# Optimization experiments

Measured on AMD Instinct MI355X. Metric: run time of the kernel, lower is better.

The kernel has to match this reference:

```python
import jax, jax.numpy as jnp
import numpy as np

B, L, IN, DM, DS, DC, EXP = 4, 1024, 256, 1024, 16, 4, 2
DI = EXP * DM            # d_inner = 2048
DTR = (DM + 15) // 16    # dt_rank = 64


def setup_inputs() -> dict:
    key = jax.random.key(0)
    ks = jax.random.split(key, 10)
    s = lambda k, sh, sc: jax.random.normal(k, sh, jnp.float32) * sc
    return {
        "x": s(ks[0], (B, L, IN), 1.0),
        "W_emb": s(ks[1], (DM, IN), IN ** -0.5),
        "b_emb": jnp.zeros((DM,), jnp.float32),
        "in_proj_w": s(ks[2], (2 * DI, DM), DM ** -0.5),
        "conv_w": s(ks[3], (DI, 1, DC), DC ** -0.5),
        "conv_b": jnp.zeros((DI,), jnp.float32),
        "x_proj_w": s(ks[4], (DTR + 2 * DS, DI), DI ** -0.5),
        "dt_proj_w": s(ks[5], (DI, DTR), DTR ** -0.5),
        "dt_proj_b": s(ks[6], (DI,), 0.1),
        "A_log": jnp.tile(jnp.log(jnp.arange(1, DS + 1, dtype=jnp.float32)), (DI, 1)),
        "D": jnp.ones((DI,), jnp.float32),
        "out_proj_w": s(ks[7], (DM, DI), DI ** -0.5),
        "fc_w": s(ks[8], (1, DM), DM ** -0.5),
        "fc_b": jnp.zeros((1,), jnp.float32),
    }


def _forward(x, W_emb, b_emb, in_proj_w, conv_w, conv_b, x_proj_w,
             dt_proj_w, dt_proj_b, A_log, D, out_proj_w, fc_w, fc_b):
    h = x @ W_emb.T + b_emb                      # [B,L,DM] input embedding
    xz = h @ in_proj_w.T                         # [B,L,2*DI]
    u, z = jnp.split(xz, 2, axis=-1)             # each [B,L,DI]
    # causal depthwise conv over time (pad left d_conv-1)
    uc = jax.lax.conv_general_dilated(
        u.transpose(0, 2, 1), conv_w, (1,), [(DC - 1, 0)],
        dimension_numbers=('NCH', 'OIH', 'NCH'), feature_group_count=DI)
    u = jax.nn.silu(uc.transpose(0, 2, 1) + conv_b)   # [B,L,DI]
    xdbl = u @ x_proj_w.T                        # [B,L,DTR+2*DS]
    dt, Bm, Cm = jnp.split(xdbl, [DTR, DTR + DS], axis=-1)
    delta = jax.nn.softplus(dt @ dt_proj_w.T + dt_proj_b)  # [B,L,DI]
    A = -jnp.exp(A_log)                          # [DI,DS]

    def step(hst, ins):
        d_t, B_t, C_t, u_t = ins                 # [B,DI],[B,DS],[B,DS],[B,DI]
        dA = jnp.exp(d_t[..., None] * A)         # [B,DI,DS]
        hst = dA * hst + (d_t * u_t)[..., None] * B_t[:, None, :]
        y = jnp.einsum('bds,bs->bd', hst, C_t)
        return hst, y

    h0 = jnp.zeros((B, DI, DS), u.dtype)
    _, ys = jax.lax.scan(step, h0, (delta.transpose(1, 0, 2),
                                    Bm.transpose(1, 0, 2),
                                    Cm.transpose(1, 0, 2),
                                    u.transpose(1, 0, 2)))
    y = ys.transpose(1, 0, 2) + D * u            # [B,L,DI] with D skip
    y = y * jax.nn.silu(z)                       # gate
    out = y @ out_proj_w.T                       # [B,L,DM]
    return out[:, -1, :] @ fc_w.T + fc_b         # [B,1]


def reference(x, W_emb, b_emb, in_proj_w, conv_w, conv_b, x_proj_w,
              dt_proj_w, dt_proj_b, A_log, D, out_proj_w, fc_w, fc_b):
    return _forward(x, W_emb, b_emb, in_proj_w, conv_w, conv_b, x_proj_w,
                    dt_proj_w, dt_proj_b, A_log, D, out_proj_w, fc_w, fc_b)
```

## Files before the change

kernel.cpp:

```cpp
#include <hip/hip_runtime.h>
#include <cstddef>
#include <cstdint>

namespace {

typedef _Float16 half8 __attribute__((ext_vector_type(8)));
typedef _Float16 half4 __attribute__((ext_vector_type(4)));
typedef float f32x4 __attribute__((ext_vector_type(4)));

constexpr int Bn   = 4;
constexpr int Ln   = 1024;
constexpr int INn  = 256;
constexpr int DMn  = 1024;
constexpr int DSn  = 16;
constexpr int DCn  = 4;
constexpr int DIn  = 2048;
constexpr int DTRn = 64;
constexpr int XPW  = DTRn + DSn;
constexpr int NCHUNK = 64;
constexpr int CHUNK  = Ln / NCHUNK;
constexpr int WCH  = 32;
constexpr int ML   = Bn * Ln;

__device__ __forceinline__ float silu_(float x) { return x / (1.f + __expf(-x)); }
__device__ __forceinline__ float softplus_(float x) {
    return fmaxf(x, 0.f) + __logf(1.f + __expf(-fabsf(x)));
}

__global__ __launch_bounds__(256)
void prep_mega(const float* __restrict__ x, _Float16* __restrict__ xh,
               const float* __restrict__ ip, _Float16* __restrict__ iph,
               const float* __restrict__ dtw, _Float16* __restrict__ dtwh,
               const float* __restrict__ W_emb, _Float16* __restrict__ W_embT,
               const float* __restrict__ x_proj, _Float16* __restrict__ xp_h,
               const float* __restrict__ fc_w, const float* __restrict__ out_w,
               float* __restrict__ wp,
               const float* __restrict__ b_emb, float* __restrict__ badd,
               const float* __restrict__ fc_b, float* __restrict__ out) {
    __shared__ float tile[32][33];
    const int bid = blockIdx.x, tid = threadIdx.x;
    if (bid < 4096) {
        const int n = bid;
        const float4 v = ((const float4*)ip)[n * 256 + tid];
        ((half4*)iph)[n * 256 + tid] =
            half4{(_Float16)v.x, (_Float16)v.y, (_Float16)v.z, (_Float16)v.w};
        const float4 bv = ((const float4*)b_emb)[tid];
        float s = v.x * bv.x + v.y * bv.y + v.z * bv.z + v.w * bv.w;
        for (int off = 32; off > 0; off >>= 1) s += __shfl_down(s, off);
        if ((tid & 63) == 0) tile[0][tid >> 6] = s;
        __syncthreads();
        if (tid == 0) badd[n] = tile[0][0] + tile[0][1] + tile[0][2] + tile[0][3];
    } else if (bid < 5248) {
        const float* in; _Float16* outp; int i;
        if (bid < 5120) { in = x;   outp = xh;   i = (bid - 4096) * 256 + tid; }
        else            { in = dtw; outp = dtwh; i = (bid - 5120) * 256 + tid; }
        const float4 v = ((const float4*)in)[i];
        ((half4*)outp)[i] = half4{(_Float16)v.x, (_Float16)v.y, (_Float16)v.z, (_Float16)v.w};
    } else if (bid < 5504) {
        const int bx = bid - 5248;
        const int m0 = (bx & 31) * 32, c0 = (bx >> 5) * 32;
        const int lc = tid & 31, lr = tid >> 5;
        #pragma unroll
        for (int ph = 0; ph < 4; ++ph)
            tile[lr + ph * 8][lc] = W_emb[(size_t)(m0 + lr + ph * 8) * INn + c0 + lc];
        __syncthreads();
        #pragma unroll
        for (int ph = 0; ph < 4; ++ph)
            W_embT[(size_t)(c0 + lr + ph * 8) * DMn + m0 + lc] = (_Float16)tile[lc][lr + ph * 8];
    } else if (bid < 5760) {
        const int i = (bid - 5504) * 256 + tid;
        const int r = i >> 9;
        const int c4 = i & 511;
        half4 h;
        if (r < XPW) {
            const float4 v = ((const float4*)(x_proj + (size_t)r * DIn))[c4];
            h = half4{(_Float16)v.x, (_Float16)v.y, (_Float16)v.z, (_Float16)v.w};
        } else {
            h = half4{(_Float16)0.f, (_Float16)0.f, (_Float16)0.f, (_Float16)0.f};
        }
        ((half4*)(xp_h + (size_t)r * DIn))[c4] = h;
    } else if (bid < 6016) {
        const int bx = bid - 5760;
        const int d = (bx & 7) * 256 + tid;
        const int c = bx >> 3;
        const int mstep = DMn / WCH;
        float s = 0.f;
        for (int m = c * mstep; m < (c + 1) * mstep; ++m)
            s += fc_w[m] * out_w[(size_t)m * DIn + d];
        wp[(size_t)c * DIn + d] = s;
    } else {
        if (tid < Bn) out[tid] = fc_b[0];
    }
}

__global__ __launch_bounds__(256)
void skgemm2(const _Float16* __restrict__ A, int lda,
             const _Float16* __restrict__ Bw, int ldb,
             float* __restrict__ P, int N, int Kc) {
    __shared__ _Float16 As[128 * 32];
    __shared__ _Float16 Bs[128 * 32];
    const int tid  = threadIdx.x;
    const int lane = tid & 63, wid = tid >> 6;
    const int wm = wid >> 1, wn = wid & 1;
    const int sk = blockIdx.x;
    const int m0 = blockIdx.y * 128;
    const int n0 = blockIdx.z * 128;
    const int M  = gridDim.y * 128;

    f32x4 acc[4][4] = {};
    const int kbeg = sk * Kc;
    for (int k0 = kbeg; k0 < kbeg + Kc; k0 += 32) {
        #pragma unroll
        for (int i = 0; i < 2; ++i) {
            const int off = tid * 16 + i * 4096;
            const int row = off >> 6;
            const int ch  = (off & 63) >> 1;
            const _Float16* ga = A  + (size_t)(m0 + row) * lda + k0 + ch;
            const _Float16* gb = Bw + (size_t)(n0 + row) * ldb + k0 + ch;
            __builtin_amdgcn_global_load_lds(
                (const __attribute__((address_space(1))) void*)ga,
                (__attribute__((address_space(3))) void*)(&As[off >> 1]), 16, 0, 0);
            __builtin_amdgcn_global_load_lds(
                (const __attribute__((address_space(1))) void*)gb,
                (__attribute__((address_space(3))) void*)(&Bs[off >> 1]), 16, 0, 0);
        }
        __syncthreads();
        const int ar = lane & 15;
        const int kq = (lane >> 4) * 8;
        half8 af[4], bf[4];
        #pragma unroll
        for (int i = 0; i < 4; ++i)
            af[i] = *(const half8*)&As[(wm * 64 + i * 16 + ar) * 32 + kq];
        #pragma unroll
        for (int j = 0; j < 4; ++j)
            bf[j] = *(const half8*)&Bs[(wn * 64 + j * 16 + ar) * 32 + kq];
        #pragma unroll
        for (int i = 0; i < 4; ++i)
            #pragma unroll
            for (int j = 0; j < 4; ++j)
                acc[i][j] = __builtin_amdgcn_mfma_f32_16x16x32_f16(af[i], bf[j], acc[i][j], 0, 0, 0);
        __syncthreads();
    }

    const int cr = (lane >> 4) * 4;
    const int cn = lane & 15;
    #pragma unroll
    for (int i = 0; i < 4; ++i) {
        #pragma unroll
        for (int j = 0; j < 4; ++j) {
            const int n = n0 + wn * 64 + j * 16 + cn;
            if (n < N) {
                #pragma unroll
                for (int r = 0; r < 4; ++r) {
                    const int m = m0 + wm * 64 + i * 16 + cr + r;
                    P[((size_t)sk * M + m) * N + n] = acc[i][j][r];
                }
            }
        }
    }
}

__global__ __launch_bounds__(256)
void skcomb(const float* __restrict__ P, _Float16* __restrict__ out, int total, int nsk) {
    const int i = blockIdx.x * 256 + threadIdx.x;
    if (i >= total) return;
    float s = 0.f;
    for (int k = 0; k < nsk; ++k) s += P[(size_t)k * total + i];
    out[i] = (_Float16)s;
}

__global__ __launch_bounds__(256)
void skcombB_clast(const float* __restrict__ P, _Float16* __restrict__ dtBh,
                   const _Float16* __restrict__ u, const float* __restrict__ x_proj,
                   float* __restrict__ Clast) {
    const int bid = blockIdx.x, tid = threadIdx.x;
    if (bid < 1280) {
        const int i = bid * 256 + tid;
        float s = 0.f;
        #pragma unroll
        for (int k = 0; k < 8; ++k) s += P[(size_t)k * (ML * XPW) + i];
        dtBh[i] = (_Float16)s;
    } else {
        const int wave = tid >> 6, lane = tid & 63;
        const int task = (bid - 1280) * 4 + wave;
        const int s_idx = task & 15, b = task >> 4;
        const _Float16* ur = u + ((size_t)b * Ln + (Ln - 1)) * DIn;
        const float* w = x_proj + (size_t)(XPW + s_idx) * DIn;
        float s = 0.f;
        for (int k = lane; k < DIn; k += 64) s += (float)ur[k] * w[k];
        for (int off = 32; off > 0; off >>= 1) s += __shfl_down(s, off);
        if (lane == 0) Clast[b * DSn + s_idx] = s;
    }
}

template<int ACT, bool HAS_BIAS>
__global__ __launch_bounds__(256)
void hgemm(const _Float16* __restrict__ A, int lda,
           const _Float16* __restrict__ Bw, int ldb,
           const float* __restrict__ bias,
           _Float16* __restrict__ Ch, int ldc,
           int N, int K) {
    __shared__ _Float16 As[128 * 32];
    __shared__ _Float16 Bs[128 * 32];
    const int tid  = threadIdx.x;
    const int lane = tid & 63, wid = tid >> 6;
    const int wm = wid >> 1, wn = wid & 1;
    const int m0 = blockIdx.y * 128, n0 = blockIdx.x * 128;

    f32x4 acc[4][4] = {};

    for (int k0 = 0; k0 < K; k0 += 32) {
        #pragma unroll
        for (int i = 0; i < 2; ++i) {
            const int off = tid * 16 + i * 4096;
            const int row = off >> 6;
            const int ch  = (off & 63) >> 1;
            const _Float16* ga = A  + (size_t)(m0 + row) * lda + k0 + ch;
            const _Float16* gb = Bw + (size_t)(n0 + row) * ldb + k0 + ch;
            __builtin_amdgcn_global_load_lds(
                (const __attribute__((address_space(1))) void*)ga,
                (__attribute__((address_space(3))) void*)(&As[off >> 1]), 16, 0, 0);
            __builtin_amdgcn_global_load_lds(
                (const __attribute__((address_space(1))) void*)gb,
                (__attribute__((address_space(3))) void*)(&Bs[off >> 1]), 16, 0, 0);
        }
        __syncthreads();

        const int ar = lane & 15;
        const int kq = (lane >> 4) * 8;
        half8 af[4], bf[4];
        #pragma unroll
        for (int i = 0; i < 4; ++i)
            af[i] = *(const half8*)&As[(wm * 64 + i * 16 + ar) * 32 + kq];
        #pragma unroll
        for (int j = 0; j < 4; ++j)
            bf[j] = *(const half8*)&Bs[(wn * 64 + j * 16 + ar) * 32 + kq];
        #pragma unroll
        for (int i = 0; i < 4; ++i)
            #pragma unroll
            for (int j = 0; j < 4; ++j)
                acc[i][j] = __builtin_amdgcn_mfma_f32_16x16x32_f16(af[i], bf[j], acc[i][j], 0, 0, 0);
        __syncthreads();
    }

    const int cr = (lane >> 4) * 4;
    const int cn = lane & 15;
    #pragma unroll
    for (int i = 0; i < 4; ++i) {
        #pragma unroll
        for (int j = 0; j < 4; ++j) {
            const int n = n0 + wn * 64 + j * 16 + cn;
            if (n < N) {
                #pragma unroll
                for (int r = 0; r < 4; ++r) {
                    const int m = m0 + wm * 64 + i * 16 + cr + r;
                    float v = acc[i][j][r];
                    if (HAS_BIAS) v += bias[n];
                    if (ACT == 1) v = softplus_(v);
                    Ch[(size_t)m * ldc + n] = (_Float16)v;
                }
            }
        }
    }
}

__global__ __launch_bounds__(256)
void conv_zlast(const _Float16* __restrict__ upre, const float* __restrict__ cw,
                const float* __restrict__ cb, _Float16* __restrict__ uh,
                const float* __restrict__ x, const _Float16* __restrict__ Wfh,
                const float* __restrict__ badd, float* __restrict__ zlast) {
    const int tid = threadIdx.x;
    const int bid = blockIdx.x;
    if (bid < 1024) {
        const int b  = bid >> 8;
        const int t0 = (bid & 255) * 4;
        const int d0 = tid * 8;
        const size_t rowbase = ((size_t)b * Ln + t0) * DIn + d0;

        half8 hzero;
        #pragma unroll
        for (int q = 0; q < 8; ++q) hzero[q] = (_Float16)0.f;

        half8 rows[7];
        if (t0 >= 3) {
            #pragma unroll
            for (int r = 0; r < 7; ++r)
                rows[r] = *(const half8*)(upre + rowbase + (ptrdiff_t)(r - 3) * DIn);
        } else {
            #pragma unroll
            for (int r = 0; r < 7; ++r) {
                const int t = t0 - 3 + r;
                rows[r] = (t >= 0) ? *(const half8*)(upre + rowbase + (ptrdiff_t)(r - 3) * DIn) : hzero;
            }
        }

        f32x4 cwq[8];
        float cbv[8];
        #pragma unroll
        for (int q = 0; q < 8; ++q) {
            cwq[q] = *(const f32x4*)(cw + (size_t)(d0 + q) * DCn);
            cbv[q] = cb[d0 + q];
        }

        #pragma unroll
        for (int s = 0; s < 4; ++s) {
            half8 o;
            #pragma unroll
            for (int q = 0; q < 8; ++q) {
                float acc = cbv[q];
                #pragma unroll
                for (int j = 0; j < DCn; ++j) acc += (float)rows[s + j][q] * cwq[q][j];
                o[q] = (_Float16)silu_(acc);
            }
            *(half8*)(uh + rowbase + (size_t)s * DIn) = o;
        }
    } else {
        const int task = (bid - 1024) * 256 + tid;
        const int j = task & (DIn - 1), b = task >> 11;
        const float4* x4 = (const float4*)(x + ((size_t)b * Ln + (Ln - 1)) * INn);
        const half4* w4 = (const half4*)(Wfh + (size_t)(DIn + j) * INn);
        float s = 0.f;
        #pragma unroll 8
        for (int q = 0; q < 64; ++q) {
            const float4 xv = x4[q];
            const half4 wv = w4[q];
            s += (float)wv[0] * xv.x + (float)wv[1] * xv.y
               + (float)wv[2] * xv.z + (float)wv[3] * xv.w;
        }
        zlast[(size_t)b * DIn + j] = s + badd[DIn + j];
    }
}

__global__ __launch_bounds__(256)
void scan_chunk_kernel(const _Float16* __restrict__ delta, const _Float16* __restrict__ u,
                       const _Float16* __restrict__ dtBh, const float* __restrict__ A_log,
                       float* __restrict__ cS, _Float16* __restrict__ cH) {
    const int d = blockIdx.x * 256 + threadIdx.x;
    const int c = blockIdx.y, b = blockIdx.z;
    float A[DSn], h[DSn];
    const float4* al = (const float4*)(A_log + (size_t)d * DSn);
    #pragma unroll
    for (int q = 0; q < 4; ++q) {
        const float4 v = al[q];
        A[q * 4 + 0] = -__expf(v.x); A[q * 4 + 1] = -__expf(v.y);
        A[q * 4 + 2] = -__expf(v.z); A[q * 4 + 3] = -__expf(v.w);
        h[q * 4 + 0] = 0.f; h[q * 4 + 1] = 0.f; h[q * 4 + 2] = 0.f; h[q * 4 + 3] = 0.f;
    }
    const float A0 = A[0];
    bool structured = true;
    #pragma unroll
    for (int s = 1; s < DSn; ++s)
        structured = structured && (fabsf(A[s] - (float)(s + 1) * A0) <= 1e-4f * (s + 1));

    float Ssum = 0.f;
    const size_t base = ((size_t)b * Ln + (size_t)c * CHUNK) * DIn + d;
    const _Float16* Bp = dtBh + ((size_t)b * Ln + (size_t)c * CHUNK) * XPW + DTRn;
    if (structured) {
        #pragma unroll 4
        for (int tt = 0; tt < CHUNK; ++tt) {
            const float dl = (float)delta[base + (size_t)tt * DIn];
            const float uu = (float)u[base + (size_t)tt * DIn];
            const float du = dl * uu;
            Ssum += dl;
            const half8 bv0 = *(const half8*)(Bp + tt * XPW);
            const half8 bv1 = *(const half8*)(Bp + tt * XPW + 8);
            float Bv[DSn];
            #pragma unroll
            for (int q = 0; q < 8; ++q) { Bv[q] = (float)bv0[q]; Bv[8 + q] = (float)bv1[q]; }
            const float e1 = __expf(dl * A0);
            const float e2 = e1 * e1, e4 = e2 * e2, e8 = e4 * e4;
            float E[DSn];
            E[0] = e1;      E[1] = e2;      E[2] = e2 * e1;  E[3] = e4;
            E[4] = e4 * e1; E[5] = e4 * e2; E[6] = E[5] * e1; E[7] = e8;
            E[8] = e8 * e1; E[9] = e8 * e2; E[10] = E[9] * e1; E[11] = e8 * e4;
            E[12] = E[11] * e1; E[13] = E[11] * e2; E[14] = E[13] * e1; E[15] = e8 * e8;
            #pragma unroll
            for (int s = 0; s < DSn; ++s) h[s] = E[s] * h[s] + du * Bv[s];
        }
    } else {
        #pragma unroll 4
        for (int tt = 0; tt < CHUNK; ++tt) {
            const float dl = (float)delta[base + (size_t)tt * DIn];
            const float uu = (float)u[base + (size_t)tt * DIn];
            const float du = dl * uu;
            Ssum += dl;
            const half8 bv0 = *(const half8*)(Bp + tt * XPW);
            const half8 bv1 = *(const half8*)(Bp + tt * XPW + 8);
            float Bv[DSn];
            #pragma unroll
            for (int q = 0; q < 8; ++q) { Bv[q] = (float)bv0[q]; Bv[8 + q] = (float)bv1[q]; }
            #pragma unroll
            for (int s = 0; s < DSn; ++s) h[s] = __expf(dl * A[s]) * h[s] + du * Bv[s];
        }
    }
    const size_t cidx = ((size_t)b * NCHUNK + c) * DIn + d;
    cS[cidx] = Ssum;
    half8 o0, o1;
    #pragma unroll
    for (int q = 0; q < 8; ++q) { o0[q] = (_Float16)h[q]; o1[q] = (_Float16)h[8 + q]; }
    *(half8*)(cH + cidx * DSn) = o0;
    *(half8*)(cH + cidx * DSn + 8) = o1;
}

__global__ __launch_bounds__(256)
void combine_v3(const float* __restrict__ cS, const _Float16* __restrict__ cH,
                const float* __restrict__ A_log, const float* __restrict__ Clast,
                const float* __restrict__ Dp, const _Float16* __restrict__ u,
                const float* __restrict__ zlast, const float* __restrict__ wp,
                float* __restrict__ out) {
    __shared__ float acc[16];
    const int tid = threadIdx.x;
    const int s = tid & 15;
    const int d = blockIdx.x * 16 + (tid >> 4);
    const int b = blockIdx.y;
    const float A = -__expf(A_log[(size_t)d * DSn + s]);
    float h = 0.f;
    const size_t cb0 = (size_t)b * NCHUNK;
    for (int c = 0; c < NCHUNK; ++c) {
        const size_t cidx = (cb0 + c) * DIn + d;
        h = __expf(A * cS[cidx]) * h + (float)cH[cidx * DSn + s];
    }
    float y = h * Clast[b * DSn + s];
    y += __shfl_xor(y, 1);
    y += __shfl_xor(y, 2);
    y += __shfl_xor(y, 4);
    y += __shfl_xor(y, 8);
    if (s == 0) {
        const float ul = (float)u[((size_t)b * Ln + (Ln - 1)) * DIn + d];
        float yy = y + Dp[d] * ul;
        yy *= silu_(zlast[(size_t)b * DIn + d]);
        float w = 0.f;
        #pragma unroll
        for (int c = 0; c < WCH; ++c) w += wp[(size_t)c * DIn + d];
        acc[tid >> 4] = yy * w;
    }
    __syncthreads();
    if (tid == 0) {
        float t = 0.f;
        #pragma unroll
        for (int i = 0; i < 16; ++i) t += acc[i];
        atomicAdd(&out[b], t);
    }
}

}

extern "C" void kernel_launch(void* const* d_in, const int* in_sizes, int n_in,
                              void* d_out, int out_size, void* d_ws, size_t ws_size,
                              hipStream_t stream) {
    (void)in_sizes; (void)n_in; (void)out_size; (void)ws_size;
    const float* x       = (const float*)d_in[0];
    const float* W_emb   = (const float*)d_in[1];
    const float* b_emb   = (const float*)d_in[2];
    const float* in_proj = (const float*)d_in[3];
    const float* conv_w  = (const float*)d_in[4];
    const float* conv_b  = (const float*)d_in[5];
    const float* x_proj  = (const float*)d_in[6];
    const float* dt_w    = (const float*)d_in[7];
    const float* dt_b    = (const float*)d_in[8];
    const float* A_log   = (const float*)d_in[9];
    const float* Dp      = (const float*)d_in[10];
    const float* out_w   = (const float*)d_in[11];
    const float* fc_w    = (const float*)d_in[12];
    const float* fc_b    = (const float*)d_in[13];
    float* out = (float*)d_out;
    char* w8 = (char*)d_ws;

    const size_t MB = 1ull << 20;
    _Float16* upreh    = (_Float16*)(w8);
    _Float16* uh       = (_Float16*)(w8 + 16 * MB);
    float*    wfoldP   = (float*)(w8 + 32 * MB);
    _Float16* deltah   = (_Float16*)(w8 + 32 * MB);
    float*    skp      = (float*)(w8 + 48 * MB);
    float*    cS       = skp;
    _Float16* cH       = (_Float16*)(w8 + 50 * MB);
    _Float16* dtBh     = (_Float16*)(w8 + 67 * MB);
    _Float16* xh       = (_Float16*)(w8 + 68 * MB);
    _Float16* W_embT_h = (_Float16*)(w8 + 70 * MB);
    _Float16* in_projh = (_Float16*)(w8 + 71 * MB);
    _Float16* xp_h     = (_Float16*)(w8 + 79 * MB);
    _Float16* dt_wh    = (_Float16*)(w8 + 80 * MB);
    _Float16* Wfoldh   = (_Float16*)(w8 + 81 * MB);
    float*    wp       = (float*)(w8 + 83 * MB);
    float*    badd     = (float*)(w8 + 84 * MB);
    float*    zlast    = badd + 4096;
    float*    Clast    = zlast + (size_t)Bn * DIn;

    prep_mega<<<6017, 256, 0, stream>>>(x, xh, in_proj, in_projh, dt_w, dt_wh,
                                        W_emb, W_embT_h, x_proj, xp_h,
                                        fc_w, out_w, wp, b_emb, badd, fc_b, out);

    skgemm2<<<dim3(4, ML / 128, 2), 256, 0, stream>>>(
        in_projh, DMn, W_embT_h, DMn, wfoldP, INn, 256);
    skcomb<<<(ML * INn + 255) / 256, 256, 0, stream>>>(wfoldP, Wfoldh, ML * INn, 4);

    hgemm<0, true><<<dim3(DIn / 128, ML / 128), 256, 0, stream>>>(
        xh, INn, Wfoldh, INn, badd, upreh, DIn, DIn, INn);
    conv_zlast<<<1056, 256, 0, stream>>>(upreh, conv_w, conv_b, uh, x, Wfoldh, badd, zlast);
    skgemm2<<<dim3(8, ML / 128, 1), 256, 0, stream>>>(uh, DIn, xp_h, DIn, skp, XPW, 256);
    skcombB_clast<<<1296, 256, 0, stream>>>(skp, dtBh, uh, x_proj, Clast);
    hgemm<1, true><<<dim3(DIn / 128, ML / 128), 256, 0, stream>>>(
        dtBh, XPW, dt_wh, DTRn, dt_b, deltah, DIn, DIn, DTRn);
    scan_chunk_kernel<<<dim3(DIn / 256, NCHUNK, Bn), 256, 0, stream>>>(
        deltah, uh, dtBh, A_log, cS, cH);
    combine_v3<<<dim3(DIn / 16, Bn), 256, 0, stream>>>(
        cS, cH, A_log, Clast, Dp, uh, zlast, wp, out);
}
```

Before: 127.4 us.

## Fuse split-K combine, Clast dot and dt_proj softplus GEMM into one kernel

Replaces the separate split-K reduction kernel (skcombB_clast) and the dt_proj hgemm with one kernel, delta_fused. Each of 128 GEMM blocks reduces the 8 split-K partials for its 128 rows straight into LDS, then loops over 4 N-tiles of dt_proj and applies bias and softplus. Sixteen extra blocks compute the C vector for the last timestep. This removes a launch and the round trip of dtBh through memory before the GEMM. In exchange, the GEMM runs on only 128 blocks instead of 512, and the partial sums are read redundantly by the 4 N-groups.

```diff
diff --git a/kernel.cpp b/kernel.cpp
--- a/kernel.cpp
+++ b/kernel.cpp
@@ -115,13 +115,11 @@
             const int off = tid * 16 + i * 4096;
             const int row = off >> 6;
             const int ch  = (off & 63) >> 1;
-            const _Float16* ga = A  + (size_t)(m0 + row) * lda + k0 + ch;
-            const _Float16* gb = Bw + (size_t)(n0 + row) * ldb + k0 + ch;
             __builtin_amdgcn_global_load_lds(
-                (const __attribute__((address_space(1))) void*)ga,
+                (const __attribute__((address_space(1))) void*)(A + (size_t)(m0 + row) * lda + k0 + ch),
                 (__attribute__((address_space(3))) void*)(&As[off >> 1]), 16, 0, 0);
             __builtin_amdgcn_global_load_lds(
-                (const __attribute__((address_space(1))) void*)gb,
+                (const __attribute__((address_space(1))) void*)(Bw + (size_t)(n0 + row) * ldb + k0 + ch),
                 (__attribute__((address_space(3))) void*)(&Bs[off >> 1]), 16, 0, 0);
         }
         __syncthreads();
@@ -141,11 +139,10 @@
                 acc[i][j] = __builtin_amdgcn_mfma_f32_16x16x32_f16(af[i], bf[j], acc[i][j], 0, 0, 0);
         __syncthreads();
     }
-
     const int cr = (lane >> 4) * 4;
     const int cn = lane & 15;
     #pragma unroll
-    for (int i = 0; i < 4; ++i) {
+    for (int i = 0; i < 4; ++i)
         #pragma unroll
         for (int j = 0; j < 4; ++j) {
             const int n = n0 + wn * 64 + j * 16 + cn;
@@ -157,7 +154,6 @@
                 }
             }
         }
-    }
 }
 
 __global__ __launch_bounds__(256)
@@ -167,30 +163,6 @@
     float s = 0.f;
     for (int k = 0; k < nsk; ++k) s += P[(size_t)k * total + i];
     out[i] = (_Float16)s;
-}
-
-__global__ __launch_bounds__(256)
-void skcombB_clast(const float* __restrict__ P, _Float16* __restrict__ dtBh,
-                   const _Float16* __restrict__ u, const float* __restrict__ x_proj,
-                   float* __restrict__ Clast) {
-    const int bid = blockIdx.x, tid = threadIdx.x;
-    if (bid < 1280) {
-        const int i = bid * 256 + tid;
-        float s = 0.f;
-        #pragma unroll
-        for (int k = 0; k < 8; ++k) s += P[(size_t)k * (ML * XPW) + i];
-        dtBh[i] = (_Float16)s;
-    } else {
-        const int wave = tid >> 6, lane = tid & 63;
-        const int task = (bid - 1280) * 4 + wave;
-        const int s_idx = task & 15, b = task >> 4;
-        const _Float16* ur = u + ((size_t)b * Ln + (Ln - 1)) * DIn;
-        const float* w = x_proj + (size_t)(XPW + s_idx) * DIn;
-        float s = 0.f;
-        for (int k = lane; k < DIn; k += 64) s += (float)ur[k] * w[k];
-        for (int off = 32; off > 0; off >>= 1) s += __shfl_down(s, off);
-        if (lane == 0) Clast[b * DSn + s_idx] = s;
-    }
 }
 
 template<int ACT, bool HAS_BIAS>
@@ -208,24 +180,20 @@
     const int m0 = blockIdx.y * 128, n0 = blockIdx.x * 128;
 
     f32x4 acc[4][4] = {};
-
     for (int k0 = 0; k0 < K; k0 += 32) {
         #pragma unroll
         for (int i = 0; i < 2; ++i) {
             const int off = tid * 16 + i * 4096;
             const int row = off >> 6;
             const int ch  = (off & 63) >> 1;
-            const _Float16* ga = A  + (size_t)(m0 + row) * lda + k0 + ch;
-            const _Float16* gb = Bw + (size_t)(n0 + row) * ldb + k0 + ch;
             __builtin_amdgcn_global_load_lds(
-                (const __attribute__((address_space(1))) void*)ga,
+                (const __attribute__((address_space(1))) void*)(A + (size_t)(m0 + row) * lda + k0 + ch),
                 (__attribute__((address_space(3))) void*)(&As[off >> 1]), 16, 0, 0);
             __builtin_amdgcn_global_load_lds(
-                (const __attribute__((address_space(1))) void*)gb,
+                (const __attribute__((address_space(1))) void*)(Bw + (size_t)(n0 + row) * ldb + k0 + ch),
                 (__attribute__((address_space(3))) void*)(&Bs[off >> 1]), 16, 0, 0);
         }
         __syncthreads();
-
         const int ar = lane & 15;
         const int kq = (lane >> 4) * 8;
         half8 af[4], bf[4];
@@ -242,11 +210,10 @@
                 acc[i][j] = __builtin_amdgcn_mfma_f32_16x16x32_f16(af[i], bf[j], acc[i][j], 0, 0, 0);
         __syncthreads();
     }
-
     const int cr = (lane >> 4) * 4;
     const int cn = lane & 15;
     #pragma unroll
-    for (int i = 0; i < 4; ++i) {
+    for (int i = 0; i < 4; ++i)
         #pragma unroll
         for (int j = 0; j < 4; ++j) {
             const int n = n0 + wn * 64 + j * 16 + cn;
@@ -261,7 +228,6 @@
                 }
             }
         }
-    }
 }
 
 __global__ __launch_bounds__(256)
@@ -276,11 +242,9 @@
         const int t0 = (bid & 255) * 4;
         const int d0 = tid * 8;
         const size_t rowbase = ((size_t)b * Ln + t0) * DIn + d0;
-
         half8 hzero;
         #pragma unroll
         for (int q = 0; q < 8; ++q) hzero[q] = (_Float16)0.f;
-
         half8 rows[7];
         if (t0 >= 3) {
             #pragma unroll
@@ -293,7 +257,6 @@
                 rows[r] = (t >= 0) ? *(const half8*)(upre + rowbase + (ptrdiff_t)(r - 3) * DIn) : hzero;
             }
         }
-
         f32x4 cwq[8];
         float cbv[8];
         #pragma unroll
@@ -301,7 +264,6 @@
             cwq[q] = *(const f32x4*)(cw + (size_t)(d0 + q) * DCn);
             cbv[q] = cb[d0 + q];
         }
-
         #pragma unroll
         for (int s = 0; s < 4; ++s) {
             half8 o;
@@ -315,8 +277,8 @@
             *(half8*)(uh + rowbase + (size_t)s * DIn) = o;
         }
     } else {
-        const int task = (bid - 1024) * 256 + tid;
-        const int j = task & (DIn - 1), b = task >> 11;
+        const int t = (bid - 1024) * 256 + tid;
+        const int j = t & (DIn - 1), b = t >> 11;
         const float4* x4 = (const float4*)(x + ((size_t)b * Ln + (Ln - 1)) * INn);
         const half4* w4 = (const half4*)(Wfh + (size_t)(DIn + j) * INn);
         float s = 0.f;
@@ -328,6 +290,119 @@
                + (float)wv[2] * xv.z + (float)wv[3] * xv.w;
         }
         zlast[(size_t)b * DIn + j] = s + badd[DIn + j];
+    }
+}
+
+__global__ __launch_bounds__(256)
+void delta_fused(const float* __restrict__ skp, const _Float16* __restrict__ dtwh,
+                 const float* __restrict__ dt_b, _Float16* __restrict__ dtBh,
+                 _Float16* __restrict__ deltah,
+                 const _Float16* __restrict__ uh, const float* __restrict__ x_proj,
+                 float* __restrict__ Clast) {
+    const int tid = threadIdx.x;
+    const int bid = blockIdx.x;
+    if (bid >= 128) {
+        const int wave = tid >> 6, lane = tid & 63;
+        const int task = (bid - 128) * 4 + wave;
+        const int s_idx = task & 15, b = task >> 4;
+        const _Float16* ur = uh + ((size_t)b * Ln + (Ln - 1)) * DIn;
+        const float* w = x_proj + (size_t)(XPW + s_idx) * DIn;
+        float s = 0.f;
+        for (int k = lane; k < DIn; k += 64) s += (float)ur[k] * w[k];
+        for (int off = 32; off > 0; off >>= 1) s += __shfl_down(s, off);
+        if (lane == 0) Clast[b * DSn + s_idx] = s;
+        return;
+    }
+    __shared__ _Float16 As[2 * 128 * 32];
+    __shared__ _Float16 Bs[2 * 128 * 32];
+    const int mt = bid >> 2, ng = bid & 3;
+    const int m0 = mt * 128;
+
+    {
+        const int r = tid >> 1;
+        const int c0 = (tid & 1) * 40;
+        float4 s4[10];
+        #pragma unroll
+        for (int q = 0; q < 10; ++q) s4[q] = float4{0.f, 0.f, 0.f, 0.f};
+        #pragma unroll
+        for (int sk = 0; sk < 8; ++sk) {
+            const float4* src = (const float4*)(skp + (size_t)sk * (ML * XPW)
+                                                + (size_t)(m0 + r) * XPW + c0);
+            #pragma unroll
+            for (int q = 0; q < 10; ++q) {
+                const float4 v = src[q];
+                s4[q].x += v.x; s4[q].y += v.y; s4[q].z += v.z; s4[q].w += v.w;
+            }
+        }
+        #pragma unroll
+        for (int q = 0; q < 10; ++q) {
+            const int c = c0 + q * 4;
+            if (c < 64) {
+                const int base = (c >> 5) * 4096 + r * 32 + (c & 31);
+                As[base + 0] = (_Float16)s4[q].x;
+                As[base + 1] = (_Float16)s4[q].y;
+                As[base + 2] = (_Float16)s4[q].z;
+                As[base + 3] = (_Float16)s4[q].w;
+            }
+        }
+        if (ng == 0) {
+            half4* dst = (half4*)(dtBh + (size_t)(m0 + r) * XPW + c0);
+            #pragma unroll
+            for (int q = 0; q < 10; ++q)
+                dst[q] = half4{(_Float16)s4[q].x, (_Float16)s4[q].y,
+                               (_Float16)s4[q].z, (_Float16)s4[q].w};
+        }
+    }
+    __syncthreads();
+
+    const int lane = tid & 63, wid = tid >> 6;
+    const int wm = wid >> 1, wn = wid & 1;
+    const int ar = lane & 15;
+    const int kq = (lane >> 4) * 8;
+    const int cr = (lane >> 4) * 4;
+    const int cn = lane & 15;
+    for (int j = 0; j < 4; ++j) {
+        const int n0 = (ng * 4 + j) * 128;
+        #pragma unroll
+        for (int ro = 0; ro < 4; ++ro) {
+            const int e0 = (ro * 256 + tid) * 8;
+            const int ks = e0 >> 12;
+            const int rem = e0 & 4095;
+            const int rr = rem >> 5;
+            const int cc = rem & 31;
+            __builtin_amdgcn_global_load_lds(
+                (const __attribute__((address_space(1))) void*)(dtwh + (size_t)(n0 + rr) * DTRn + ks * 32 + cc),
+                (__attribute__((address_space(3))) void*)(Bs + e0), 16, 0, 0);
+        }
+        __syncthreads();
+        f32x4 acc[4][4] = {};
+        #pragma unroll
+        for (int ks = 0; ks < 2; ++ks) {
+            half8 af[4], bf[4];
+            #pragma unroll
+            for (int i = 0; i < 4; ++i)
+                af[i] = *(const half8*)(As + ks * 4096 + (wm * 64 + i * 16 + ar) * 32 + kq);
+            #pragma unroll
+            for (int jj = 0; jj < 4; ++jj)
+                bf[jj] = *(const half8*)(Bs + ks * 4096 + (wn * 64 + jj * 16 + ar) * 32 + kq);
+            #pragma unroll
+            for (int i = 0; i < 4; ++i)
+                #pragma unroll
+                for (int jj = 0; jj < 4; ++jj)
+                    acc[i][jj] = __builtin_amdgcn_mfma_f32_16x16x32_f16(af[i], bf[jj], acc[i][jj], 0, 0, 0);
+        }
+        #pragma unroll
+        for (int i = 0; i < 4; ++i)
+            #pragma unroll
+            for (int jj = 0; jj < 4; ++jj) {
+                const int n = n0 + wn * 64 + jj * 16 + cn;
+                #pragma unroll
+                for (int r2 = 0; r2 < 4; ++r2) {
+                    const int m = m0 + wm * 64 + i * 16 + cr + r2;
+                    deltah[(size_t)m * DIn + n] = (_Float16)softplus_(acc[i][jj][r2] + dt_b[n]);
+                }
+            }
+        __syncthreads();
     }
 }
 
@@ -351,7 +426,6 @@
     #pragma unroll
     for (int s = 1; s < DSn; ++s)
         structured = structured && (fabsf(A[s] - (float)(s + 1) * A0) <= 1e-4f * (s + 1));
-
     float Ssum = 0.f;
     const size_t base = ((size_t)b * Ln + (size_t)c * CHUNK) * DIn + d;
     const _Float16* Bp = dtBh + ((size_t)b * Ln + (size_t)c * CHUNK) * XPW + DTRn;
@@ -489,18 +563,14 @@
     prep_mega<<<6017, 256, 0, stream>>>(x, xh, in_proj, in_projh, dt_w, dt_wh,
                                         W_emb, W_embT_h, x_proj, xp_h,
                                         fc_w, out_w, wp, b_emb, badd, fc_b, out);
-
     skgemm2<<<dim3(4, ML / 128, 2), 256, 0, stream>>>(
         in_projh, DMn, W_embT_h, DMn, wfoldP, INn, 256);
     skcomb<<<(ML * INn + 255) / 256, 256, 0, stream>>>(wfoldP, Wfoldh, ML * INn, 4);
-
     hgemm<0, true><<<dim3(DIn / 128, ML / 128), 256, 0, stream>>>(
         xh, INn, Wfoldh, INn, badd, upreh, DIn, DIn, INn);
     conv_zlast<<<1056, 256, 0, stream>>>(upreh, conv_w, conv_b, uh, x, Wfoldh, badd, zlast);
     skgemm2<<<dim3(8, ML / 128, 1), 256, 0, stream>>>(uh, DIn, xp_h, DIn, skp, XPW, 256);
-    skcombB_clast<<<1296, 256, 0, stream>>>(skp, dtBh, uh, x_proj, Clast);
-    hgemm<1, true><<<dim3(DIn / 128, ML / 128), 256, 0, stream>>>(
-        dtBh, XPW, dt_wh, DTRn, dt_b, deltah, DIn, DIn, DTRn);
+    delta_fused<<<144, 256, 0, stream>>>(skp, dt_wh, dt_b, dtBh, deltah, uh, x_proj, Clast);
     scan_chunk_kernel<<<dim3(DIn / 256, NCHUNK, Bn), 256, 0, stream>>>(
         deltah, uh, dtBh, A_log, cS, cH);
     combine_v3<<<dim3(DIn / 16, Bn), 256, 0, stream>>>(
```

New measurement: 152.3 us. 19.6% more time.

## Fuse delta projection GEMM with softplus into chunked scan kernel via LDS

Applied to the files above, without the earlier changes.

Merges the dt_proj GEMM (with bias and softplus) and the chunked selective-scan kernel into one kernel. The delta tile stays in shared memory, so the fp16 delta tensor is no longer written to and re-read from global memory, and one launch goes away. The B values for the tile are staged into LDS as well. The generic templated hgemm is also specialised into a fixed-shape upre GEMM. The cost is that each block now runs only 256 threads over 8 chunks in two rounds, which lowers scan parallelism compared with the old grid, and it uses more shared memory per block.

```diff
diff --git a/kernel.cpp b/kernel.cpp
--- a/kernel.cpp
+++ b/kernel.cpp
@@ -115,13 +115,11 @@
             const int off = tid * 16 + i * 4096;
             const int row = off >> 6;
             const int ch  = (off & 63) >> 1;
-            const _Float16* ga = A  + (size_t)(m0 + row) * lda + k0 + ch;
-            const _Float16* gb = Bw + (size_t)(n0 + row) * ldb + k0 + ch;
             __builtin_amdgcn_global_load_lds(
-                (const __attribute__((address_space(1))) void*)ga,
+                (const __attribute__((address_space(1))) void*)(A + (size_t)(m0 + row) * lda + k0 + ch),
                 (__attribute__((address_space(3))) void*)(&As[off >> 1]), 16, 0, 0);
             __builtin_amdgcn_global_load_lds(
-                (const __attribute__((address_space(1))) void*)gb,
+                (const __attribute__((address_space(1))) void*)(Bw + (size_t)(n0 + row) * ldb + k0 + ch),
                 (__attribute__((address_space(3))) void*)(&Bs[off >> 1]), 16, 0, 0);
         }
         __syncthreads();
@@ -141,11 +139,10 @@
                 acc[i][j] = __builtin_amdgcn_mfma_f32_16x16x32_f16(af[i], bf[j], acc[i][j], 0, 0, 0);
         __syncthreads();
     }
-
     const int cr = (lane >> 4) * 4;
     const int cn = lane & 15;
     #pragma unroll
-    for (int i = 0; i < 4; ++i) {
+    for (int i = 0; i < 4; ++i)
         #pragma unroll
         for (int j = 0; j < 4; ++j) {
             const int n = n0 + wn * 64 + j * 16 + cn;
@@ -157,7 +154,6 @@
                 }
             }
         }
-    }
 }
 
 __global__ __launch_bounds__(256)
@@ -193,13 +189,9 @@
     }
 }
 
-template<int ACT, bool HAS_BIAS>
-__global__ __launch_bounds__(256)
-void hgemm(const _Float16* __restrict__ A, int lda,
-           const _Float16* __restrict__ Bw, int ldb,
-           const float* __restrict__ bias,
-           _Float16* __restrict__ Ch, int ldc,
-           int N, int K) {
+__global__ __launch_bounds__(256)
+void hgemm_upre(const _Float16* __restrict__ A, const _Float16* __restrict__ Bw,
+                const float* __restrict__ bias, _Float16* __restrict__ Ch) {
     __shared__ _Float16 As[128 * 32];
     __shared__ _Float16 Bs[128 * 32];
     const int tid  = threadIdx.x;
@@ -208,24 +200,20 @@
     const int m0 = blockIdx.y * 128, n0 = blockIdx.x * 128;
 
     f32x4 acc[4][4] = {};
-
-    for (int k0 = 0; k0 < K; k0 += 32) {
+    for (int k0 = 0; k0 < INn; k0 += 32) {
         #pragma unroll
         for (int i = 0; i < 2; ++i) {
             const int off = tid * 16 + i * 4096;
             const int row = off >> 6;
             const int ch  = (off & 63) >> 1;
-            const _Float16* ga = A  + (size_t)(m0 + row) * lda + k0 + ch;
-            const _Float16* gb = Bw + (size_t)(n0 + row) * ldb + k0 + ch;
             __builtin_amdgcn_global_load_lds(
-                (const __attribute__((address_space(1))) void*)ga,
+                (const __attribute__((address_space(1))) void*)(A + (size_t)(m0 + row) * INn + k0 + ch),
                 (__attribute__((address_space(3))) void*)(&As[off >> 1]), 16, 0, 0);
             __builtin_amdgcn_global_load_lds(
-                (const __attribute__((address_space(1))) void*)gb,
+                (const __attribute__((address_space(1))) void*)(Bw + (size_t)(n0 + row) * INn + k0 + ch),
                 (__attribute__((address_space(3))) void*)(&Bs[off >> 1]), 16, 0, 0);
         }
         __syncthreads();
-
         const int ar = lane & 15;
         const int kq = (lane >> 4) * 8;
         half8 af[4], bf[4];
@@ -242,26 +230,19 @@
                 acc[i][j] = __builtin_amdgcn_mfma_f32_16x16x32_f16(af[i], bf[j], acc[i][j], 0, 0, 0);
         __syncthreads();
     }
-
     const int cr = (lane >> 4) * 4;
     const int cn = lane & 15;
     #pragma unroll
-    for (int i = 0; i < 4; ++i) {
+    for (int i = 0; i < 4; ++i)
         #pragma unroll
         for (int j = 0; j < 4; ++j) {
             const int n = n0 + wn * 64 + j * 16 + cn;
-            if (n < N) {
-                #pragma unroll
-                for (int r = 0; r < 4; ++r) {
-                    const int m = m0 + wm * 64 + i * 16 + cr + r;
-                    float v = acc[i][j][r];
-                    if (HAS_BIAS) v += bias[n];
-                    if (ACT == 1) v = softplus_(v);
-                    Ch[(size_t)m * ldc + n] = (_Float16)v;
-                }
-            }
-        }
-    }
+            #pragma unroll
+            for (int r = 0; r < 4; ++r) {
+                const int m = m0 + wm * 64 + i * 16 + cr + r;
+                Ch[(size_t)m * DIn + n] = (_Float16)(acc[i][j][r] + bias[n]);
+            }
+        }
 }
 
 __global__ __launch_bounds__(256)
@@ -276,11 +257,9 @@
         const int t0 = (bid & 255) * 4;
         const int d0 = tid * 8;
         const size_t rowbase = ((size_t)b * Ln + t0) * DIn + d0;
-
         half8 hzero;
         #pragma unroll
         for (int q = 0; q < 8; ++q) hzero[q] = (_Float16)0.f;
-
         half8 rows[7];
         if (t0 >= 3) {
             #pragma unroll
@@ -293,7 +272,6 @@
                 rows[r] = (t >= 0) ? *(const half8*)(upre + rowbase + (ptrdiff_t)(r - 3) * DIn) : hzero;
             }
         }
-
         f32x4 cwq[8];
         float cbv[8];
         #pragma unroll
@@ -301,7 +279,6 @@
             cwq[q] = *(const f32x4*)(cw + (size_t)(d0 + q) * DCn);
             cbv[q] = cb[d0 + q];
         }
-
         #pragma unroll
         for (int s = 0; s < 4; ++s) {
             half8 o;
@@ -315,8 +292,8 @@
             *(half8*)(uh + rowbase + (size_t)s * DIn) = o;
         }
     } else {
-        const int task = (bid - 1024) * 256 + tid;
-        const int j = task & (DIn - 1), b = task >> 11;
+        const int t = (bid - 1024) * 256 + tid;
+        const int j = t & (DIn - 1), b = t >> 11;
         const float4* x4 = (const float4*)(x + ((size_t)b * Ln + (Ln - 1)) * INn);
         const half4* w4 = (const half4*)(Wfh + (size_t)(DIn + j) * INn);
         float s = 0.f;
@@ -332,19 +309,86 @@
 }
 
 __global__ __launch_bounds__(256)
-void scan_chunk_kernel(const _Float16* __restrict__ delta, const _Float16* __restrict__ u,
-                       const _Float16* __restrict__ dtBh, const float* __restrict__ A_log,
-                       float* __restrict__ cS, _Float16* __restrict__ cH) {
-    const int d = blockIdx.x * 256 + threadIdx.x;
-    const int c = blockIdx.y, b = blockIdx.z;
-    float A[DSn], h[DSn];
-    const float4* al = (const float4*)(A_log + (size_t)d * DSn);
-    #pragma unroll
-    for (int q = 0; q < 4; ++q) {
-        const float4 v = al[q];
-        A[q * 4 + 0] = -__expf(v.x); A[q * 4 + 1] = -__expf(v.y);
-        A[q * 4 + 2] = -__expf(v.z); A[q * 4 + 3] = -__expf(v.w);
-        h[q * 4 + 0] = 0.f; h[q * 4 + 1] = 0.f; h[q * 4 + 2] = 0.f; h[q * 4 + 3] = 0.f;
+void delta_scan(const _Float16* __restrict__ dtBh, const _Float16* __restrict__ dtwh,
+                const float* __restrict__ dt_b, const _Float16* __restrict__ uh,
+                const float* __restrict__ A_log,
+                float* __restrict__ cS, _Float16* __restrict__ cH) {
+    __shared__ _Float16 As[128 * 32];
+    __shared__ _Float16 Bs[128 * 32];
+    __shared__ _Float16 Ds[128][132];
+    const int tid = threadIdx.x;
+    const int lane = tid & 63, wid = tid >> 6;
+    const int wm = wid >> 1, wn = wid & 1;
+    const int m0 = blockIdx.y * 128, n0 = blockIdx.x * 128;
+
+    f32x4 acc[4][4] = {};
+    for (int k0 = 0; k0 < DTRn; k0 += 32) {
+        #pragma unroll
+        for (int i = 0; i < 2; ++i) {
+            const int off = tid * 16 + i * 4096;
+            const int row = off >> 6;
+            const int ch  = (off & 63) >> 1;
+            __builtin_amdgcn_global_load_lds(
+                (const __attribute__((address_space(1))) void*)(dtBh + (size_t)(m0 + row) * XPW + k0 + ch),
+                (__attribute__((address_space(3))) void*)(&As[off >> 1]), 16, 0, 0);
+            __builtin_amdgcn_global_load_lds(
+                (const __attribute__((address_space(1))) void*)(dtwh + (size_t)(n0 + row) * DTRn + k0 + ch),
+                (__attribute__((address_space(3))) void*)(&Bs[off >> 1]), 16, 0, 0);
+        }
+        __syncthreads();
+        const int ar = lane & 15;
+        const int kq = (lane >> 4) * 8;
+        half8 af[4], bf[4];
+        #pragma unroll
+        for (int i = 0; i < 4; ++i)
+            af[i] = *(const half8*)&As[(wm * 64 + i * 16 + ar) * 32 + kq];
+        #pragma unroll
+        for (int j = 0; j < 4; ++j)
+            bf[j] = *(const half8*)&Bs[(wn * 64 + j * 16 + ar) * 32 + kq];
+        #pragma unroll
+        for (int i = 0; i < 4; ++i)
+            #pragma unroll
+            for (int j = 0; j < 4; ++j)
+                acc[i][j] = __builtin_amdgcn_mfma_f32_16x16x32_f16(af[i], bf[j], acc[i][j], 0, 0, 0);
+        __syncthreads();
+    }
+
+    {
+        const int row = tid >> 1, off = (tid & 1) * 8;
+        *(half8*)&Bs[row * 16 + off] =
+            *(const half8*)(dtBh + (size_t)(m0 + row) * XPW + 64 + off);
+    }
+    {
+        const int cr = (lane >> 4) * 4;
+        const int cn = lane & 15;
+        #pragma unroll
+        for (int i = 0; i < 4; ++i)
+            #pragma unroll
+            for (int j = 0; j < 4; ++j) {
+                const int ln = wn * 64 + j * 16 + cn;
+                const float bb = dt_b[n0 + ln];
+                #pragma unroll
+                for (int r = 0; r < 4; ++r) {
+                    const int lm = wm * 64 + i * 16 + cr + r;
+                    Ds[lm][ln] = (_Float16)softplus_(acc[i][j][r] + bb);
+                }
+            }
+    }
+    __syncthreads();
+
+    const int bb = m0 >> 10;
+    const int tb = m0 & 1023;
+    const int dcol = tid & 127;
+    const int d = n0 + dcol;
+    float A[DSn];
+    {
+        const float4* al = (const float4*)(A_log + (size_t)d * DSn);
+        #pragma unroll
+        for (int q = 0; q < 4; ++q) {
+            const float4 v = al[q];
+            A[q * 4 + 0] = -__expf(v.x); A[q * 4 + 1] = -__expf(v.y);
+            A[q * 4 + 2] = -__expf(v.z); A[q * 4 + 3] = -__expf(v.w);
+        }
     }
     const float A0 = A[0];
     bool structured = true;
@@ -352,54 +396,59 @@
     for (int s = 1; s < DSn; ++s)
         structured = structured && (fabsf(A[s] - (float)(s + 1) * A0) <= 1e-4f * (s + 1));
 
-    float Ssum = 0.f;
-    const size_t base = ((size_t)b * Ln + (size_t)c * CHUNK) * DIn + d;
-    const _Float16* Bp = dtBh + ((size_t)b * Ln + (size_t)c * CHUNK) * XPW + DTRn;
-    if (structured) {
-        #pragma unroll 4
-        for (int tt = 0; tt < CHUNK; ++tt) {
-            const float dl = (float)delta[base + (size_t)tt * DIn];
-            const float uu = (float)u[base + (size_t)tt * DIn];
-            const float du = dl * uu;
-            Ssum += dl;
-            const half8 bv0 = *(const half8*)(Bp + tt * XPW);
-            const half8 bv1 = *(const half8*)(Bp + tt * XPW + 8);
-            float Bv[DSn];
-            #pragma unroll
-            for (int q = 0; q < 8; ++q) { Bv[q] = (float)bv0[q]; Bv[8 + q] = (float)bv1[q]; }
-            const float e1 = __expf(dl * A0);
-            const float e2 = e1 * e1, e4 = e2 * e2, e8 = e4 * e4;
-            float E[DSn];
-            E[0] = e1;      E[1] = e2;      E[2] = e2 * e1;  E[3] = e4;
-            E[4] = e4 * e1; E[5] = e4 * e2; E[6] = E[5] * e1; E[7] = e8;
-            E[8] = e8 * e1; E[9] = e8 * e2; E[10] = E[9] * e1; E[11] = e8 * e4;
-            E[12] = E[11] * e1; E[13] = E[11] * e2; E[14] = E[13] * e1; E[15] = e8 * e8;
-            #pragma unroll
-            for (int s = 0; s < DSn; ++s) h[s] = E[s] * h[s] + du * Bv[s];
-        }
-    } else {
-        #pragma unroll 4
-        for (int tt = 0; tt < CHUNK; ++tt) {
-            const float dl = (float)delta[base + (size_t)tt * DIn];
-            const float uu = (float)u[base + (size_t)tt * DIn];
-            const float du = dl * uu;
-            Ssum += dl;
-            const half8 bv0 = *(const half8*)(Bp + tt * XPW);
-            const half8 bv1 = *(const half8*)(Bp + tt * XPW + 8);
-            float Bv[DSn];
-            #pragma unroll
-            for (int q = 0; q < 8; ++q) { Bv[q] = (float)bv0[q]; Bv[8 + q] = (float)bv1[q]; }
-            #pragma unroll
-            for (int s = 0; s < DSn; ++s) h[s] = __expf(dl * A[s]) * h[s] + du * Bv[s];
-        }
-    }
-    const size_t cidx = ((size_t)b * NCHUNK + c) * DIn + d;
-    cS[cidx] = Ssum;
-    half8 o0, o1;
-    #pragma unroll
-    for (int q = 0; q < 8; ++q) { o0[q] = (_Float16)h[q]; o1[q] = (_Float16)h[8 + q]; }
-    *(half8*)(cH + cidx * DSn) = o0;
-    *(half8*)(cH + cidx * DSn + 8) = o1;
+    for (int ci = (tid >> 7); ci < 8; ci += 2) {
+        float h[DSn];
+        #pragma unroll
+        for (int s = 0; s < DSn; ++s) h[s] = 0.f;
+        float Ssum = 0.f;
+        const size_t ubase = ((size_t)bb * Ln + tb + ci * 16) * DIn + d;
+        if (structured) {
+            for (int tt = 0; tt < CHUNK; ++tt) {
+                const int lr = ci * 16 + tt;
+                const float dl = (float)Ds[lr][dcol];
+                const float uu = (float)uh[ubase + (size_t)tt * DIn];
+                const float du = dl * uu;
+                Ssum += dl;
+                const half8 bv0 = *(const half8*)&Bs[lr * 16];
+                const half8 bv1 = *(const half8*)&Bs[lr * 16 + 8];
+                float Bv[DSn];
+                #pragma unroll
+                for (int q = 0; q < 8; ++q) { Bv[q] = (float)bv0[q]; Bv[8 + q] = (float)bv1[q]; }
+                const float e1 = __expf(dl * A0);
+                const float e2 = e1 * e1, e4 = e2 * e2, e8 = e4 * e4;
+                float E[DSn];
+                E[0] = e1;      E[1] = e2;      E[2] = e2 * e1;  E[3] = e4;
+                E[4] = e4 * e1; E[5] = e4 * e2; E[6] = E[5] * e1; E[7] = e8;
+                E[8] = e8 * e1; E[9] = e8 * e2; E[10] = E[9] * e1; E[11] = e8 * e4;
+                E[12] = E[11] * e1; E[13] = E[11] * e2; E[14] = E[13] * e1; E[15] = e8 * e8;
+                #pragma unroll
+                for (int s = 0; s < DSn; ++s) h[s] = E[s] * h[s] + du * Bv[s];
+            }
+        } else {
+            for (int tt = 0; tt < CHUNK; ++tt) {
+                const int lr = ci * 16 + tt;
+                const float dl = (float)Ds[lr][dcol];
+                const float uu = (float)uh[ubase + (size_t)tt * DIn];
+                const float du = dl * uu;
+                Ssum += dl;
+                const half8 bv0 = *(const half8*)&Bs[lr * 16];
+                const half8 bv1 = *(const half8*)&Bs[lr * 16 + 8];
+                float Bv[DSn];
+                #pragma unroll
+                for (int q = 0; q < 8; ++q) { Bv[q] = (float)bv0[q]; Bv[8 + q] = (float)bv1[q]; }
+                #pragma unroll
+                for (int s = 0; s < DSn; ++s) h[s] = __expf(dl * A[s]) * h[s] + du * Bv[s];
+            }
+        }
+        const int c = (tb >> 4) + ci;
+        const size_t cidx = ((size_t)bb * NCHUNK + c) * DIn + d;
+        cS[cidx] = Ssum;
+        half8 o0, o1;
+        #pragma unroll
+        for (int q = 0; q < 8; ++q) { o0[q] = (_Float16)h[q]; o1[q] = (_Float16)h[8 + q]; }
+        *(half8*)(cH + cidx * DSn) = o0;
+        *(half8*)(cH + cidx * DSn + 8) = o1;
+    }
 }
 
 __global__ __launch_bounds__(256)
@@ -470,7 +519,6 @@
     _Float16* upreh    = (_Float16*)(w8);
     _Float16* uh       = (_Float16*)(w8 + 16 * MB);
     float*    wfoldP   = (float*)(w8 + 32 * MB);
-    _Float16* deltah   = (_Float16*)(w8 + 32 * MB);
     float*    skp      = (float*)(w8 + 48 * MB);
     float*    cS       = skp;
     _Float16* cH       = (_Float16*)(w8 + 50 * MB);
@@ -489,20 +537,15 @@
     prep_mega<<<6017, 256, 0, stream>>>(x, xh, in_proj, in_projh, dt_w, dt_wh,
                                         W_emb, W_embT_h, x_proj, xp_h,
                                         fc_w, out_w, wp, b_emb, badd, fc_b, out);
-
     skgemm2<<<dim3(4, ML / 128, 2), 256, 0, stream>>>(
         in_projh, DMn, W_embT_h, DMn, wfoldP, INn, 256);
     skcomb<<<(ML * INn + 255) / 256, 256, 0, stream>>>(wfoldP, Wfoldh, ML * INn, 4);
-
-    hgemm<0, true><<<dim3(DIn / 128, ML / 128), 256, 0, stream>>>(
-        xh, INn, Wfoldh, INn, badd, upreh, DIn, DIn, INn);
+    hgemm_upre<<<dim3(DIn / 128, ML / 128), 256, 0, stream>>>(xh, Wfoldh, badd, upreh);
     conv_zlast<<<1056, 256, 0, stream>>>(upreh, conv_w, conv_b, uh, x, Wfoldh, badd, zlast);
     skgemm2<<<dim3(8, ML / 128, 1), 256, 0, stream>>>(uh, DIn, xp_h, DIn, skp, XPW, 256);
     skcombB_clast<<<1296, 256, 0, stream>>>(skp, dtBh, uh, x_proj, Clast);
-    hgemm<1, true><<<dim3(DIn / 128, ML / 128), 256, 0, stream>>>(
-        dtBh, XPW, dt_wh, DTRn, dt_b, deltah, DIn, DIn, DTRn);
-    scan_chunk_kernel<<<dim3(DIn / 256, NCHUNK, Bn), 256, 0, stream>>>(
-        deltah, uh, dtBh, A_log, cS, cH);
+    delta_scan<<<dim3(DIn / 128, ML / 128), 256, 0, stream>>>(
+        dtBh, dt_wh, dt_b, uh, A_log, cS, cH);
     combine_v3<<<dim3(DIn / 16, Bn), 256, 0, stream>>>(
         cS, cH, A_log, Clast, Dp, uh, zlast, wp, out);
 }
```

After: 130.2 us. 2.2% more time.
